# Performance work log

Hardware: AMD Instinct MI355X
Metric: run time of the kernel (lower is better)

## Reference

```python
import jax, jax.numpy as jnp
import numpy as np

N_NODES = 100000
N_EDGES = 1600000
D = 64


def setup_inputs() -> dict:
    key = jax.random.key(0)
    ks = jax.random.split(key, 9)
    x = jax.random.normal(ks[0], (N_NODES, D), dtype=jnp.float32)
    src = jax.random.randint(ks[1], (N_EDGES,), 0, N_NODES, dtype=jnp.int64)
    dst = jax.random.randint(ks[2], (N_EDGES,), 0, N_NODES, dtype=jnp.int64)
    s = 1.0 / np.sqrt(D)
    W_self1 = jax.random.normal(ks[3], (D, D), dtype=jnp.float32) * s
    W_neigh1 = jax.random.normal(ks[4], (D, D), dtype=jnp.float32) * s
    b1 = jnp.zeros((D,), dtype=jnp.float32)
    W_self2 = jax.random.normal(ks[5], (D, D), dtype=jnp.float32) * s
    W_neigh2 = jax.random.normal(ks[6], (D, D), dtype=jnp.float32) * s
    b2 = jnp.zeros((D,), dtype=jnp.float32)
    return {"x": x, "src": src, "dst": dst,
            "W_self1": W_self1, "W_neigh1": W_neigh1, "b1": b1,
            "W_self2": W_self2, "W_neigh2": W_neigh2, "b2": b2}


def _sage_layer(h, src, dst, W_self, W_neigh, b, n_nodes):
    # gather source-node features along edges: [E, d]
    msg = h[src]
    # sum messages into destination nodes, then normalize by in-degree (mean agg)
    agg = jax.ops.segment_sum(msg, dst, num_segments=n_nodes)
    deg = jax.ops.segment_sum(jnp.ones((src.shape[0], 1), h.dtype), dst,
                              num_segments=n_nodes)
    h_neigh = agg / jnp.maximum(deg, 1.0)
    # DGL SAGEConv (mean): fc_self(h) + fc_neigh(h_neigh) + bias
    return h @ W_self + h_neigh @ W_neigh + b


def reference(x, src, dst, W_self1, W_neigh1, b1, W_self2, W_neigh2, b2):
    n = x.shape[0]
    h = _sage_layer(x, src, dst, W_self1, W_neigh1, b1, n)
    # note: source module's forward applies no activation between layers
    h = _sage_layer(h, src, dst, W_self2, W_neigh2, b2, n)
    return h
```

## Files before the change

### kernel.cpp

```cpp
#include <hip/hip_runtime.h>
#include <hip/hip_bf16.h>


#define D 64
#define CAP 64
#define BNODES 256
#define BCAP 4736
#define MAXNB 512

typedef __bf16 bf16x8 __attribute__((ext_vector_type(8)));
typedef float  f32x4  __attribute__((ext_vector_type(4)));

__device__ __forceinline__ unsigned pack2(float a, float b) {
    __hip_bfloat162 t = __float22bfloat162_rn(make_float2(a, b));
    return *(unsigned*)&t;
}
__device__ __forceinline__ unsigned short f2b(float f) {
    __hip_bfloat16 b = __float2bfloat16(f);
    return *(unsigned short*)&b;
}


__global__ void __launch_bounds__(256)
prep_kernel(const float4* __restrict__ x, uint4* __restrict__ xb4,
            unsigned* __restrict__ xsent, unsigned* __restrict__ h1sent,
            const int* __restrict__ src, const int* __restrict__ dst,
            int* __restrict__ gcur, int* __restrict__ gbucket,
            int E, int NB, int n8, int bin_blocks) {
    const int bid = blockIdx.x;
    const int t   = threadIdx.x;

    if (bid < bin_blocks) {
        __shared__ int hist[MAXNB];
        for (int i = t; i < NB; i += 256) hist[i] = 0;
        __syncthreads();

        const int e4_total = E >> 2;
        const int base4    = bid * 1024;

        int4 sv[4], dv[4];
        bool have[4];
        #pragma unroll
        for (int k = 0; k < 4; ++k) {
            int i4 = base4 + t + k * 256;
            have[k] = i4 < e4_total;
            if (have[k]) {
                sv[k] = ((const int4*)src)[i4];
                dv[k] = ((const int4*)dst)[i4];
            }
        }

        #pragma unroll
        for (int k = 0; k < 4; ++k) if (have[k]) {
            atomicAdd(&hist[dv[k].x >> 8], 1);
            atomicAdd(&hist[dv[k].y >> 8], 1);
            atomicAdd(&hist[dv[k].z >> 8], 1);
            atomicAdd(&hist[dv[k].w >> 8], 1);
        }

        int  tail_s = 0, tail_d = 0;
        bool have_tail = false;
        if (bid == 0) {
            int e = (e4_total << 2) + t;
            if (e < E) {
                tail_s = src[e]; tail_d = dst[e]; have_tail = true;
                atomicAdd(&hist[tail_d >> 8], 1);
            }
        }
        __syncthreads();

        for (int i = t; i < NB; i += 256) {
            int c = hist[i];
            hist[i] = (c > 0) ? atomicAdd(&gcur[i], c) : 0;
        }
        __syncthreads();

        #pragma unroll
        for (int k = 0; k < 4; ++k) if (have[k]) {
            int4 s = sv[k], d = dv[k];
            int b, p;
            b = d.x >> 8; p = atomicAdd(&hist[b], 1); if (p < BCAP) gbucket[b * BCAP + p] = ((d.x & 255) << 17) | s.x;
            b = d.y >> 8; p = atomicAdd(&hist[b], 1); if (p < BCAP) gbucket[b * BCAP + p] = ((d.y & 255) << 17) | s.y;
            b = d.z >> 8; p = atomicAdd(&hist[b], 1); if (p < BCAP) gbucket[b * BCAP + p] = ((d.z & 255) << 17) | s.z;
            b = d.w >> 8; p = atomicAdd(&hist[b], 1); if (p < BCAP) gbucket[b * BCAP + p] = ((d.w & 255) << 17) | s.w;
        }
        if (have_tail) {
            int b = tail_d >> 8, p = atomicAdd(&hist[b], 1);
            if (p < BCAP) gbucket[b * BCAP + p] = ((tail_d & 255) << 17) | tail_s;
        }
        return;
    }

    const int cb = bid - bin_blocks;
    const int i  = cb * 256 + t;
    if (i < n8) {
        float4 a = x[2 * i], b = x[2 * i + 1];
        uint4 o;
        o.x = pack2(a.x, a.y);
        o.y = pack2(a.z, a.w);
        o.z = pack2(b.x, b.y);
        o.w = pack2(b.z, b.w);
        xb4[i] = o;
    }
    if (cb == 0 && t < 64) {
        if (t < 32) xsent[t] = 0u;
        else        h1sent[t - 32] = 0u;
    }
}


__global__ void __launch_bounds__(256)
ellify_kernel(const int* __restrict__ gcur, const int* __restrict__ gbucket,
              int* __restrict__ cnt, int* __restrict__ edge_idx, int N) {
    __shared__ int scnt[BNODES];
    scnt[threadIdx.x] = 0;
    __syncthreads();

    const int b     = blockIdx.x;
    const int ne    = min(gcur[b], BCAP);
    const int node0 = b << 8;

    for (int e = threadIdx.x; e < ne; e += 256) {
        int p   = gbucket[b * BCAP + e];
        int s   = p & 0x1FFFF;
        int ld  = p >> 17;
        int pos = atomicAdd(&scnt[ld], 1);
        if (pos < CAP) edge_idx[(size_t)(node0 + ld) * CAP + pos] = s;
    }
    __syncthreads();

    int node = node0 + threadIdx.x;
    if (node < N) {
        int raw = scnt[threadIdx.x];
        cnt[node] = raw;
        int c  = min(raw, CAP);
        int c8 = (c + 7) & ~7;
        for (int p = c; p < c8; ++p)
            edge_idx[(size_t)node * CAP + p] = N;
    }
}


__device__ __forceinline__ void acc8(float& a0, float& a1, float& a2, float& a3,
                                     float& a4, float& a5, float& a6, float& a7,
                                     uint4 u) {
    a0 += __uint_as_float(u.x << 16);
    a1 += __uint_as_float(u.x & 0xffff0000u);
    a2 += __uint_as_float(u.y << 16);
    a3 += __uint_as_float(u.y & 0xffff0000u);
    a4 += __uint_as_float(u.z << 16);
    a5 += __uint_as_float(u.z & 0xffff0000u);
    a6 += __uint_as_float(u.w << 16);
    a7 += __uint_as_float(u.w & 0xffff0000u);
}

__device__ __forceinline__ uint4 gather_row8(const uint4* __restrict__ h4,
                                             const int* __restrict__ cnt,
                                             const int* __restrict__ edge_idx,
                                             int node, int N, int q, int g) {
    const int count = (node < N) ? min(cnt[node], CAP) : 0;
    const int c8    = (count + 7) & ~7;
    const int start = node * CAP;
    const int b0    = g << 3;

    float a0 = 0.f, a1 = 0.f, a2 = 0.f, a3 = 0.f;
    float a4 = 0.f, a5 = 0.f, a6 = 0.f, a7 = 0.f;

    for (int j = 0; j < c8; j += 8) {
        const int sreg = edge_idx[start + j + q];
        const int s0 = __shfl(sreg, b0 + 0, 64);
        const int s1 = __shfl(sreg, b0 + 1, 64);
        const int s2 = __shfl(sreg, b0 + 2, 64);
        const int s3 = __shfl(sreg, b0 + 3, 64);
        const int s4 = __shfl(sreg, b0 + 4, 64);
        const int s5 = __shfl(sreg, b0 + 5, 64);
        const int s6 = __shfl(sreg, b0 + 6, 64);
        const int s7 = __shfl(sreg, b0 + 7, 64);
        uint4 u0 = h4[(size_t)s0 * 8 + q];
        uint4 u1 = h4[(size_t)s1 * 8 + q];
        uint4 u2 = h4[(size_t)s2 * 8 + q];
        uint4 u3 = h4[(size_t)s3 * 8 + q];
        uint4 u4 = h4[(size_t)s4 * 8 + q];
        uint4 u5 = h4[(size_t)s5 * 8 + q];
        uint4 u6 = h4[(size_t)s6 * 8 + q];
        uint4 u7 = h4[(size_t)s7 * 8 + q];
        acc8(a0, a1, a2, a3, a4, a5, a6, a7, u0);
        acc8(a0, a1, a2, a3, a4, a5, a6, a7, u1);
        acc8(a0, a1, a2, a3, a4, a5, a6, a7, u2);
        acc8(a0, a1, a2, a3, a4, a5, a6, a7, u3);
        acc8(a0, a1, a2, a3, a4, a5, a6, a7, u4);
        acc8(a0, a1, a2, a3, a4, a5, a6, a7, u5);
        acc8(a0, a1, a2, a3, a4, a5, a6, a7, u6);
        acc8(a0, a1, a2, a3, a4, a5, a6, a7, u7);
    }

    const float inv = 1.0f / fmaxf((float)count, 1.0f);
    uint4 o;
    o.x = pack2(a0 * inv, a1 * inv);
    o.y = pack2(a2 * inv, a3 * inv);
    o.z = pack2(a4 * inv, a5 * inv);
    o.w = pack2(a6 * inv, a7 * inv);
    return o;
}

__device__ __forceinline__ bf16x8 cvt8(float4 a, float4 b) {
    union { bf16x8 v; __hip_bfloat162 p[4]; } u;
    u.p[0] = __float22bfloat162_rn(make_float2(a.x, a.y));
    u.p[1] = __float22bfloat162_rn(make_float2(a.z, a.w));
    u.p[2] = __float22bfloat162_rn(make_float2(b.x, b.y));
    u.p[3] = __float22bfloat162_rn(make_float2(b.z, b.w));
    return u.v;
}
__device__ __forceinline__ bf16x8 asbf(uint4 u) {
    union { uint4 a; bf16x8 v; } c; c.a = u; return c.v;
}

__global__ void __launch_bounds__(256, 3)
fused_kernel(const unsigned short* __restrict__ h,
             const int* __restrict__ cnt,
             const int* __restrict__ edge_idx,
             const float* __restrict__ Wself,
             const float* __restrict__ Wneigh,
             const float* __restrict__ bias,
             float* __restrict__ out_f32,
             unsigned short* __restrict__ out_bf16, int N) {
    const int lane = threadIdx.x & 63;
    const int q    = lane & 7;
    const int g    = lane >> 3;
    const int col  = lane & 15;
    const int quad = lane >> 4;
    const int wave = blockIdx.x * (blockDim.x >> 6) + (threadIdx.x >> 6);
    const int n_waves = gridDim.x * (blockDim.x >> 6);

    bf16x8 Bf[4][4];
    #pragma unroll
    for (int nt = 0; nt < 4; ++nt) {
        const int n = nt * 16 + col;
        #pragma unroll
        for (int kk = 0; kk < 4; ++kk) {
            const float* W = (kk < 2) ? Wself : Wneigh;
            const int kbase = (kk & 1) * 32 + quad * 8;
            float w0 = W[(kbase + 0) * D + n];
            float w1 = W[(kbase + 1) * D + n];
            float w2 = W[(kbase + 2) * D + n];
            float w3 = W[(kbase + 3) * D + n];
            float w4 = W[(kbase + 4) * D + n];
            float w5 = W[(kbase + 5) * D + n];
            float w6 = W[(kbase + 6) * D + n];
            float w7 = W[(kbase + 7) * D + n];
            Bf[nt][kk] = cvt8(make_float4(w0, w1, w2, w3), make_float4(w4, w5, w6, w7));
        }
    }

    float bv[4];
    #pragma unroll
    for (int nt = 0; nt < 4; ++nt) bv[nt] = bias[nt * 16 + col];

    const uint4* __restrict__ h4 = (const uint4*)h;

    const int tiles = (N + 15) >> 4;
    for (int t = wave; t < tiles; t += n_waves) {
        uint4 P0 = gather_row8(h4, cnt, edge_idx, t * 16 + g,     N, q, g);

        int row = t * 16 + col;
        if (row >= N) row = N - 1;
        uint4 A0u = h4[(size_t)row * 8 + quad];
        uint4 A1u = h4[(size_t)row * 8 + 4 + quad];

        uint4 P1 = gather_row8(h4, cnt, edge_idx, t * 16 + 8 + g, N, q, g);

        const int srcA2 = ((lane & 7) << 3) + quad;
        const int srcA3 = srcA2 + 4;
        const bool hi   = (lane & 8) != 0;
        uint4 A2u, A3u;
        {
            unsigned l0 = __shfl(P0.x, srcA2, 64), h0 = __shfl(P1.x, srcA2, 64);
            unsigned l1 = __shfl(P0.y, srcA2, 64), h1 = __shfl(P1.y, srcA2, 64);
            unsigned l2 = __shfl(P0.z, srcA2, 64), h2 = __shfl(P1.z, srcA2, 64);
            unsigned l3 = __shfl(P0.w, srcA2, 64), h3 = __shfl(P1.w, srcA2, 64);
            A2u.x = hi ? h0 : l0;  A2u.y = hi ? h1 : l1;
            A2u.z = hi ? h2 : l2;  A2u.w = hi ? h3 : l3;
        }
        {
            unsigned l0 = __shfl(P0.x, srcA3, 64), h0 = __shfl(P1.x, srcA3, 64);
            unsigned l1 = __shfl(P0.y, srcA3, 64), h1 = __shfl(P1.y, srcA3, 64);
            unsigned l2 = __shfl(P0.z, srcA3, 64), h2 = __shfl(P1.z, srcA3, 64);
            unsigned l3 = __shfl(P0.w, srcA3, 64), h3 = __shfl(P1.w, srcA3, 64);
            A3u.x = hi ? h0 : l0;  A3u.y = hi ? h1 : l1;
            A3u.z = hi ? h2 : l2;  A3u.w = hi ? h3 : l3;
        }

        bf16x8 A0 = asbf(A0u), A1 = asbf(A1u);
        bf16x8 A2 = asbf(A2u), A3 = asbf(A3u);

        #pragma unroll
        for (int nt = 0; nt < 4; ++nt) {
            f32x4 acc = {bv[nt], bv[nt], bv[nt], bv[nt]};
            acc = __builtin_amdgcn_mfma_f32_16x16x32_bf16(A0, Bf[nt][0], acc, 0, 0, 0);
            acc = __builtin_amdgcn_mfma_f32_16x16x32_bf16(A1, Bf[nt][1], acc, 0, 0, 0);
            acc = __builtin_amdgcn_mfma_f32_16x16x32_bf16(A2, Bf[nt][2], acc, 0, 0, 0);
            acc = __builtin_amdgcn_mfma_f32_16x16x32_bf16(A3, Bf[nt][3], acc, 0, 0, 0);
            if (out_f32) {
                #pragma unroll
                for (int r = 0; r < 4; ++r) {
                    const int orow = t * 16 + quad * 4 + r;
                    if (orow < N) out_f32[(size_t)orow * D + nt * 16 + col] = acc[r];
                }
            } else {
                #pragma unroll
                for (int r = 0; r < 4; ++r) {
                    const int orow = t * 16 + quad * 4 + r;
                    if (orow < N) out_bf16[(size_t)orow * D + nt * 16 + col] = f2b(acc[r]);
                }
            }
        }
    }
}


extern "C" void kernel_launch(void* const* d_in, const int* in_sizes, int n_in,
                              void* d_out, int out_size, void* d_ws, size_t ws_size,
                              hipStream_t stream) {
    const float* x   = (const float*)d_in[0];
    const int*   src = (const int*)d_in[1];
    const int*   dst = (const int*)d_in[2];
    const float* Ws1 = (const float*)d_in[3];
    const float* Wn1 = (const float*)d_in[4];
    const float* b1  = (const float*)d_in[5];
    const float* Ws2 = (const float*)d_in[6];
    const float* Wn2 = (const float*)d_in[7];
    const float* b2  = (const float*)d_in[8];

    const int N = in_sizes[0] / D;
    const int E = in_sizes[1];

    float* out = (float*)d_out;

    const int NB = (N + BNODES - 1) / BNODES;

    int* gcur      = (int*)d_ws;
    int* cnt       = gcur + 512;
    int* edge_idx  = cnt + N;
    unsigned short* xb   = (unsigned short*)(edge_idx + (size_t)N * CAP);
    unsigned short* h1b  = xb + (size_t)(N + 1) * D;
    int* gbucket   = (int*)(h1b + (size_t)(N + 1) * D);

    const int n8         = N * D / 8;
    const int cvt_blocks = (n8 + 255) / 256;
    const int e4_total   = E >> 2;
    const int bin_blocks = (e4_total + 1023) / 1024 > 0 ? (e4_total + 1023) / 1024 : 1;

    hipMemsetAsync(gcur, 0, 512 * sizeof(int), stream);

    prep_kernel<<<bin_blocks + cvt_blocks, 256, 0, stream>>>(
        (const float4*)x, (uint4*)xb,
        (unsigned*)(xb + (size_t)N * D), (unsigned*)(h1b + (size_t)N * D),
        src, dst, gcur, gbucket, E, NB, n8, bin_blocks);

    ellify_kernel<<<NB, 256, 0, stream>>>(gcur, gbucket, cnt, edge_idx, N);

    const int tiles  = (N + 15) / 16;
    const int fblocks = (tiles + 3) / 4;

    fused_kernel<<<fblocks, 256, 0, stream>>>(xb, cnt, edge_idx, Ws1, Wn1, b1,
                                              nullptr, h1b, N);
    fused_kernel<<<fblocks, 256, 0, stream>>>(h1b, cnt, edge_idx, Ws2, Wn2, b2,
                                              out, nullptr, N);
}
```

Baseline: 207.8 us.

## Stage weights in swizzled LDS, unroll gather by 16, use persistent grid

The bf16 weight fragments now live in a bank-swizzled shared-memory tile that each wave re-reads per tile, instead of being held in 64 VGPRs per thread. This lowers register pressure so launch bounds can ask for 4 blocks per SIMD. The neighbour gather loop is unrolled to 16 edges per iteration to keep more loads in flight. The grid becomes a fixed 1024 persistent blocks that stride over tiles, which amortises the per-block LDS fill but adds LDS reads inside the tile loop.

```diff
diff --git a/kernel.cpp b/kernel.cpp
--- a/kernel.cpp
+++ b/kernel.cpp
@@ -154,10 +154,10 @@
     a7 += __uint_as_float(u.w & 0xffff0000u);
 }
 
-__device__ __forceinline__ uint4 gather_row8(const uint4* __restrict__ h4,
-                                             const int* __restrict__ cnt,
-                                             const int* __restrict__ edge_idx,
-                                             int node, int N, int q, int g) {
+__device__ __forceinline__ uint4 gather_row(const uint4* __restrict__ h4,
+                                            const int* __restrict__ cnt,
+                                            const int* __restrict__ edge_idx,
+                                            int node, int N, int q, int g) {
     const int count = (node < N) ? min(cnt[node], CAP) : 0;
     const int c8    = (count + 7) & ~7;
     const int start = node * CAP;
@@ -166,16 +166,69 @@
     float a0 = 0.f, a1 = 0.f, a2 = 0.f, a3 = 0.f;
     float a4 = 0.f, a5 = 0.f, a6 = 0.f, a7 = 0.f;
 
-    for (int j = 0; j < c8; j += 8) {
-        const int sreg = edge_idx[start + j + q];
-        const int s0 = __shfl(sreg, b0 + 0, 64);
-        const int s1 = __shfl(sreg, b0 + 1, 64);
-        const int s2 = __shfl(sreg, b0 + 2, 64);
-        const int s3 = __shfl(sreg, b0 + 3, 64);
-        const int s4 = __shfl(sreg, b0 + 4, 64);
-        const int s5 = __shfl(sreg, b0 + 5, 64);
-        const int s6 = __shfl(sreg, b0 + 6, 64);
-        const int s7 = __shfl(sreg, b0 + 7, 64);
+    int j = 0;
+    for (; j + 16 <= c8; j += 16) {
+        const int srA = edge_idx[start + j + q];
+        const int srB = edge_idx[start + j + 8 + q];
+        const int s0  = __shfl(srA, b0 + 0, 64);
+        const int s1  = __shfl(srA, b0 + 1, 64);
+        const int s2  = __shfl(srA, b0 + 2, 64);
+        const int s3  = __shfl(srA, b0 + 3, 64);
+        const int s4  = __shfl(srA, b0 + 4, 64);
+        const int s5  = __shfl(srA, b0 + 5, 64);
+        const int s6  = __shfl(srA, b0 + 6, 64);
+        const int s7  = __shfl(srA, b0 + 7, 64);
+        const int s8  = __shfl(srB, b0 + 0, 64);
+        const int s9  = __shfl(srB, b0 + 1, 64);
+        const int s10 = __shfl(srB, b0 + 2, 64);
+        const int s11 = __shfl(srB, b0 + 3, 64);
+        const int s12 = __shfl(srB, b0 + 4, 64);
+        const int s13 = __shfl(srB, b0 + 5, 64);
+        const int s14 = __shfl(srB, b0 + 6, 64);
+        const int s15 = __shfl(srB, b0 + 7, 64);
+        uint4 u0  = h4[(size_t)s0  * 8 + q];
+        uint4 u1  = h4[(size_t)s1  * 8 + q];
+        uint4 u2  = h4[(size_t)s2  * 8 + q];
+        uint4 u3  = h4[(size_t)s3  * 8 + q];
+        uint4 u4  = h4[(size_t)s4  * 8 + q];
+        uint4 u5  = h4[(size_t)s5  * 8 + q];
+        uint4 u6  = h4[(size_t)s6  * 8 + q];
+        uint4 u7  = h4[(size_t)s7  * 8 + q];
+        uint4 u8  = h4[(size_t)s8  * 8 + q];
+        uint4 u9  = h4[(size_t)s9  * 8 + q];
+        uint4 u10 = h4[(size_t)s10 * 8 + q];
+        uint4 u11 = h4[(size_t)s11 * 8 + q];
+        uint4 u12 = h4[(size_t)s12 * 8 + q];
+        uint4 u13 = h4[(size_t)s13 * 8 + q];
+        uint4 u14 = h4[(size_t)s14 * 8 + q];
+        uint4 u15 = h4[(size_t)s15 * 8 + q];
+        acc8(a0, a1, a2, a3, a4, a5, a6, a7, u0);
+        acc8(a0, a1, a2, a3, a4, a5, a6, a7, u1);
+        acc8(a0, a1, a2, a3, a4, a5, a6, a7, u2);
+        acc8(a0, a1, a2, a3, a4, a5, a6, a7, u3);
+        acc8(a0, a1, a2, a3, a4, a5, a6, a7, u4);
+        acc8(a0, a1, a2, a3, a4, a5, a6, a7, u5);
+        acc8(a0, a1, a2, a3, a4, a5, a6, a7, u6);
+        acc8(a0, a1, a2, a3, a4, a5, a6, a7, u7);
+        acc8(a0, a1, a2, a3, a4, a5, a6, a7, u8);
+        acc8(a0, a1, a2, a3, a4, a5, a6, a7, u9);
+        acc8(a0, a1, a2, a3, a4, a5, a6, a7, u10);
+        acc8(a0, a1, a2, a3, a4, a5, a6, a7, u11);
+        acc8(a0, a1, a2, a3, a4, a5, a6, a7, u12);
+        acc8(a0, a1, a2, a3, a4, a5, a6, a7, u13);
+        acc8(a0, a1, a2, a3, a4, a5, a6, a7, u14);
+        acc8(a0, a1, a2, a3, a4, a5, a6, a7, u15);
+    }
+    if (j < c8) {
+        const int srA = edge_idx[start + j + q];
+        const int s0 = __shfl(srA, b0 + 0, 64);
+        const int s1 = __shfl(srA, b0 + 1, 64);
+        const int s2 = __shfl(srA, b0 + 2, 64);
+        const int s3 = __shfl(srA, b0 + 3, 64);
+        const int s4 = __shfl(srA, b0 + 4, 64);
+        const int s5 = __shfl(srA, b0 + 5, 64);
+        const int s6 = __shfl(srA, b0 + 6, 64);
+        const int s7 = __shfl(srA, b0 + 7, 64);
         uint4 u0 = h4[(size_t)s0 * 8 + q];
         uint4 u1 = h4[(size_t)s1 * 8 + q];
         uint4 u2 = h4[(size_t)s2 * 8 + q];
@@ -203,19 +256,11 @@
     return o;
 }
 
-__device__ __forceinline__ bf16x8 cvt8(float4 a, float4 b) {
-    union { bf16x8 v; __hip_bfloat162 p[4]; } u;
-    u.p[0] = __float22bfloat162_rn(make_float2(a.x, a.y));
-    u.p[1] = __float22bfloat162_rn(make_float2(a.z, a.w));
-    u.p[2] = __float22bfloat162_rn(make_float2(b.x, b.y));
-    u.p[3] = __float22bfloat162_rn(make_float2(b.z, b.w));
-    return u.v;
-}
 __device__ __forceinline__ bf16x8 asbf(uint4 u) {
     union { uint4 a; bf16x8 v; } c; c.a = u; return c.v;
 }
 
-__global__ void __launch_bounds__(256, 3)
+__global__ void __launch_bounds__(256, 4)
 fused_kernel(const unsigned short* __restrict__ h,
              const int* __restrict__ cnt,
              const int* __restrict__ edge_idx,
@@ -224,6 +269,26 @@
              const float* __restrict__ bias,
              float* __restrict__ out_f32,
              unsigned short* __restrict__ out_bf16, int N) {
+    __shared__ unsigned short wt[8192];
+
+    {
+        const int t = threadIdx.x;
+        for (int idx4 = t; idx4 < 2048; idx4 += 256) {
+            const int k    = idx4 >> 4;
+            const int col0 = (idx4 & 15) << 2;
+            const float* W = (k < 64) ? (Wself + k * 64) : (Wneigh + (k - 64) * 64);
+            float4 w = *(const float4*)(W + col0);
+            #pragma unroll
+            for (int e = 0; e < 4; ++e) {
+                const int col = col0 + e;
+                const float v = (e == 0) ? w.x : (e == 1) ? w.y : (e == 2) ? w.z : w.w;
+                const int byte = col * 256 + (((k * 2)) ^ ((col & 7) << 4));
+                wt[byte >> 1] = f2b(v);
+            }
+        }
+    }
+    __syncthreads();
+
     const int lane = threadIdx.x & 63;
     const int q    = lane & 7;
     const int g    = lane >> 3;
@@ -232,26 +297,6 @@
     const int wave = blockIdx.x * (blockDim.x >> 6) + (threadIdx.x >> 6);
     const int n_waves = gridDim.x * (blockDim.x >> 6);
 
-    bf16x8 Bf[4][4];
-    #pragma unroll
-    for (int nt = 0; nt < 4; ++nt) {
-        const int n = nt * 16 + col;
-        #pragma unroll
-        for (int kk = 0; kk < 4; ++kk) {
-            const float* W = (kk < 2) ? Wself : Wneigh;
-            const int kbase = (kk & 1) * 32 + quad * 8;
-            float w0 = W[(kbase + 0) * D + n];
-            float w1 = W[(kbase + 1) * D + n];
-            float w2 = W[(kbase + 2) * D + n];
-            float w3 = W[(kbase + 3) * D + n];
-            float w4 = W[(kbase + 4) * D + n];
-            float w5 = W[(kbase + 5) * D + n];
-            float w6 = W[(kbase + 6) * D + n];
-            float w7 = W[(kbase + 7) * D + n];
-            Bf[nt][kk] = cvt8(make_float4(w0, w1, w2, w3), make_float4(w4, w5, w6, w7));
-        }
-    }
-
     float bv[4];
     #pragma unroll
     for (int nt = 0; nt < 4; ++nt) bv[nt] = bias[nt * 16 + col];
@@ -260,14 +305,14 @@
 
     const int tiles = (N + 15) >> 4;
     for (int t = wave; t < tiles; t += n_waves) {
-        uint4 P0 = gather_row8(h4, cnt, edge_idx, t * 16 + g,     N, q, g);
+        uint4 P0 = gather_row(h4, cnt, edge_idx, t * 16 + g,     N, q, g);
 
         int row = t * 16 + col;
         if (row >= N) row = N - 1;
         uint4 A0u = h4[(size_t)row * 8 + quad];
         uint4 A1u = h4[(size_t)row * 8 + 4 + quad];
 
-        uint4 P1 = gather_row8(h4, cnt, edge_idx, t * 16 + 8 + g, N, q, g);
+        uint4 P1 = gather_row(h4, cnt, edge_idx, t * 16 + 8 + g, N, q, g);
 
         const int srcA2 = ((lane & 7) << 3) + quad;
         const int srcA3 = srcA2 + 4;
@@ -292,6 +337,20 @@
 
         bf16x8 A0 = asbf(A0u), A1 = asbf(A1u);
         bf16x8 A2 = asbf(A2u), A3 = asbf(A3u);
+
+        int base = 0;
+        asm volatile("" : "+v"(base));
+        bf16x8 Bf[4][4];
+        #pragma unroll
+        for (int nt = 0; nt < 4; ++nt) {
+            const int n = nt * 16 + col;
+            #pragma unroll
+            for (int kk = 0; kk < 4; ++kk) {
+                const int kb2  = ((kk >= 2) ? 128 : 0) + (kk & 1) * 64 + quad * 16;
+                const int byte = n * 256 + (kb2 ^ ((n & 7) << 4)) + base;
+                Bf[nt][kk] = *(const bf16x8*)((const char*)wt + byte);
+            }
+        }
 
         #pragma unroll
         for (int nt = 0; nt < 4; ++nt) {
@@ -359,8 +418,7 @@
 
     ellify_kernel<<<NB, 256, 0, stream>>>(gcur, gbucket, cnt, edge_idx, N);
 
-    const int tiles  = (N + 15) / 16;
-    const int fblocks = (tiles + 3) / 4;
+    const int fblocks = 1024;
 
     fused_kernel<<<fblocks, 256, 0, stream>>>(xb, cnt, edge_idx, Ws1, Wn1, b1,
                                               nullptr, h1b, N);
```

New measurement: 215.4 us. 3.7% more time.
